# Performance work log

Hardware: AMD Instinct MI355X
Metric: run time of the kernel (lower is better)

## Reference

```python
import jax, jax.numpy as jnp
import numpy as np

B, C_LOCAL, C_GUIDE, C2, H, W = 16, 256, 256, 256, 64, 64
MID = C2 // 2          # mlp hidden channels
CQ = C_LOCAL // 4      # offset_gen hidden channels (also = groups)
EPS = 1e-5             # BatchNorm eps (inference mode)


def _conv(x, w, pad=0, groups=1, b=None):
    out = jax.lax.conv_general_dilated(
        x, w, window_strides=(1, 1), padding=((pad, pad), (pad, pad)),
        dimension_numbers=('NCHW', 'OIHW', 'NCHW'), feature_group_count=groups)
    if b is not None:
        out = out + b[None, :, None, None]
    return out


def _bn(x, g, b, m, v):
    scale = g / jnp.sqrt(v + EPS)
    return x * scale[None, :, None, None] + (b - m * scale)[None, :, None, None]


def _grid_sample(img, grid):
    # img: [C,H,W]; grid: [H,W,2] with (x,y) in [-1,1]; bilinear, zeros padding,
    # align_corners=False (pixel = ((g+1)*size - 1)/2)
    C, Hh, Ww = img.shape
    ix = (grid[..., 0] + 1.0) * (Ww * 0.5) - 0.5
    iy = (grid[..., 1] + 1.0) * (Hh * 0.5) - 0.5
    x0 = jnp.floor(ix); y0 = jnp.floor(iy)
    x1 = x0 + 1.0;      y1 = y0 + 1.0
    wx1 = ix - x0; wx0 = 1.0 - wx1
    wy1 = iy - y0; wy0 = 1.0 - wy1

    def gather(xi, yi):
        valid = (xi >= 0) & (xi < Ww) & (yi >= 0) & (yi < Hh)
        xc = jnp.clip(xi, 0, Ww - 1).astype(jnp.int32)
        yc = jnp.clip(yi, 0, Hh - 1).astype(jnp.int32)
        return img[:, yc, xc] * valid.astype(img.dtype)[None]  # [C,H,W]

    return (gather(x0, y0) * (wx0 * wy0)[None]
            + gather(x1, y0) * (wx1 * wy0)[None]
            + gather(x0, y1) * (wx0 * wy1)[None]
            + gather(x1, y1) * (wx1 * wy1)[None])


def setup_inputs() -> dict:
    key = jax.random.key(0)
    ks = jax.random.split(key, 20)
    w = lambda k, s: jax.random.normal(k, s, jnp.float32) * 0.05
    return {
        'x_local': jax.random.normal(ks[0], (B, C_LOCAL, H, W), jnp.float32),
        'x_guide': jax.random.normal(ks[1], (B, C_GUIDE, H, W), jnp.float32),
        'w_align': w(ks[2], (C2, C_GUIDE, 1, 1)),
        'bn1_g': 1.0 + 0.1 * jax.random.normal(ks[3], (C2,), jnp.float32),
        'bn1_b': 0.1 * jax.random.normal(ks[4], (C2,), jnp.float32),
        'bn1_m': 0.1 * jax.random.normal(ks[5], (C2,), jnp.float32),
        'bn1_v': 0.5 + jax.random.uniform(ks[6], (C2,), jnp.float32),
        'w_off1': w(ks[7], (CQ, 4, 3, 3)),   # grouped: in-ch per group = C_LOCAL/CQ = 4
        'w_off2': w(ks[8], (2, CQ, 1, 1)),
        'b_off2': 0.1 * jax.random.normal(ks[9], (2,), jnp.float32),
        'w_mlp1': w(ks[10], (MID, C_LOCAL, 1, 1)),
        'bn2_g': 1.0 + 0.1 * jax.random.normal(ks[11], (MID,), jnp.float32),
        'bn2_b': 0.1 * jax.random.normal(ks[12], (MID,), jnp.float32),
        'bn2_m': 0.1 * jax.random.normal(ks[13], (MID,), jnp.float32),
        'bn2_v': 0.5 + jax.random.uniform(ks[14], (MID,), jnp.float32),
        'w_mlp2': w(ks[15], (C2, MID, 1, 1)),
    }


def reference(x_local, x_guide, w_align, bn1_g, bn1_b, bn1_m, bn1_v,
              w_off1, w_off2, b_off2, w_mlp1, bn2_g, bn2_b, bn2_m, bn2_v,
              w_mlp2):
    # align(x_guide): 1x1 conv + BN
    g = _bn(_conv(x_guide, w_align), bn1_g, bn1_b, bn1_m, bn1_v)
    # offset_gen(x_local): grouped 3x3 conv -> SiLU -> 1x1 conv (bias) -> [B,2,H,W]
    off = _conv(x_local, w_off1, pad=1, groups=CQ)
    off = _conv(jax.nn.silu(off), w_off2, b=b_off2)
    # base grid in [-1,1], (x,y) last
    ys = jnp.linspace(-1.0, 1.0, H)
    xs = jnp.linspace(-1.0, 1.0, W)
    gy, gx = jnp.meshgrid(ys, xs, indexing='ij')
    base = jnp.stack((gx, gy), axis=-1)                      # [H,W,2]
    v_grid = base[None] + off.transpose(0, 2, 3, 1) * (2.0 / max(H, W))
    g_aligned = jax.vmap(_grid_sample)(g, v_grid)            # [B,C2,H,W]
    # mlp(x_local): 1x1 conv -> BN -> GELU(exact) -> 1x1 conv
    l = _conv(x_local, w_mlp1)
    l = jax.nn.gelu(_bn(l, bn2_g, bn2_b, bn2_m, bn2_v), approximate=False)
    l = _conv(l, w_mlp2)
    return jax.nn.silu(g_aligned + l)
```

## Files before the change

### kernel.cpp

```cpp
#include <hip/hip_runtime.h>

typedef unsigned short u16;
typedef __bf16 bf16x8 __attribute__((ext_vector_type(8)));
typedef float f32x4 __attribute__((ext_vector_type(4)));
typedef u16 u16x2 __attribute__((ext_vector_type(2)));
typedef u16 u16x4 __attribute__((ext_vector_type(4)));
typedef u16 u16x8 __attribute__((ext_vector_type(8)));

#define EPS 1e-5f

__device__ __forceinline__ u16 f2bf(float f) {
  unsigned u = __builtin_bit_cast(unsigned, f);
  u += 0x7FFFu + ((u >> 16) & 1u);
  return (u16)(u >> 16);
}
__device__ __forceinline__ float bf2f(u16 h) {
  unsigned u = ((unsigned)h) << 16;
  return __builtin_bit_cast(float, u);
}

__global__ void prep_weights(
    const float* __restrict__ wa, const float* __restrict__ g1, const float* __restrict__ b1,
    const float* __restrict__ m1, const float* __restrict__ v1,
    const float* __restrict__ w1, const float* __restrict__ g2, const float* __restrict__ b2,
    const float* __restrict__ m2, const float* __restrict__ v2,
    const float* __restrict__ w2,
    u16* __restrict__ Acat, u16* __restrict__ w1_o,
    float* __restrict__ bias1, float* __restrict__ bias2) {
  int c = blockIdx.x, k = threadIdx.x;
  float s1 = g1[c] / sqrtf(v1[c] + EPS);
  if (k < 256) Acat[c * 384 + k] = f2bf(wa[c * 256 + k] * s1);
  else         Acat[c * 384 + k] = f2bf(w2[c * 128 + (k - 256)]);
  if (c < 128) {
    float s2 = g2[c] / sqrtf(v2[c] + EPS);
    if (k < 256) w1_o[c * 256 + k] = f2bf(w1[c * 256 + k] * s2);
    if (k == 256) bias2[c] = b2[c] - m2[c] * s2;
  }
  if (k == 0) bias1[c] = b1[c] - m1[c] * s1;
}

__global__ __launch_bounds__(256) void gconv_kernel(
    const float* __restrict__ xl, const float* __restrict__ w1,
    u16* __restrict__ sbuf) {
  __shared__ float tile[4][18][66];
  const int tid = threadIdx.x;
  const int band = blockIdx.x;
  const int q = blockIdx.y;
  const int b = blockIdx.z;
  const float* xb = xl + ((size_t)b * 256 + 4 * q) * 4096;
  for (int i = tid; i < 4 * 18 * 66; i += 256) {
    int ci = i / (18 * 66);
    int rem = i - ci * (18 * 66);
    int r = rem / 66, c = rem - r * 66;
    int gy = band * 16 - 1 + r, gx = c - 1;
    float v = 0.f;
    if ((unsigned)gy < 64u && (unsigned)gx < 64u)
      v = xb[(size_t)ci * 4096 + gy * 64 + gx];
    tile[ci][r][c] = v;
  }
  float wq[36];
#pragma unroll
  for (int i = 0; i < 36; ++i) wq[i] = w1[q * 36 + i];
  __syncthreads();
  const int c = tid & 63, r0 = tid >> 6;
  u16* sp = sbuf + ((size_t)(b * 64 + q)) * 4096 + band * 1024;
#pragma unroll
  for (int k = 0; k < 4; ++k) {
    int r = r0 * 4 + k;
    float s = 0.f;
#pragma unroll
    for (int ci = 0; ci < 4; ++ci)
#pragma unroll
      for (int dy = 0; dy < 3; ++dy)
#pragma unroll
        for (int dx = 0; dx < 3; ++dx)
          s += wq[ci * 9 + dy * 3 + dx] * tile[ci][r + dy][c + dx];
    sp[r * 64 + c] = f2bf(s / (1.f + __expf(-s)));
  }
}

__global__ __launch_bounds__(256) void coords_kernel(
    const u16* __restrict__ sbuf, const float* __restrict__ w2,
    const float* __restrict__ b2, float* __restrict__ coords,
    float* __restrict__ wsum) {
  __shared__ float sw2[128];
  const int tid = threadIdx.x;
  if (tid < 128) sw2[tid] = w2[tid];
  __syncthreads();
  const int b = blockIdx.y;
  const int p = blockIdx.x * 256 + tid;
  const u16* sp = sbuf + (size_t)b * 64 * 4096 + p;
  float ax = 0.f, ay = 0.f;
#pragma unroll 8
  for (int q = 0; q < 64; ++q) {
    float v = bf2f(sp[(size_t)q * 4096]);
    ax += sw2[q] * v;
    ay += sw2[64 + q] * v;
  }
  int y = p >> 6, x = p & 63;
  float ix = (64.f / 63.f) * (float)x + ax + b2[0] - 0.5f;
  float iy = (64.f / 63.f) * (float)y + ay + b2[1] - 0.5f;
  ((float2*)coords)[(size_t)b * 4096 + p] = make_float2(ix, iy);
  float x0f = floorf(ix), y0f = floorf(iy);
  int x0 = (int)x0f, y0 = (int)y0f;
  float wx1 = ix - x0f, wx0 = 1.f - wx1;
  float wy1 = iy - y0f, wy0 = 1.f - wy1;
  bool vx0 = (unsigned)x0 < 64u, vx1 = (unsigned)(x0 + 1) < 64u;
  bool vy0 = (unsigned)y0 < 64u, vy1 = (unsigned)(y0 + 1) < 64u;
  float s = (vx0 && vy0 ? wx0 * wy0 : 0.f) + (vx1 && vy0 ? wx1 * wy0 : 0.f) +
            (vx0 && vy1 ? wx0 * wy1 : 0.f) + (vx1 && vy1 ? wx1 * wy1 : 0.f);
  wsum[(size_t)b * 4096 + p] = s;
}

__global__ __launch_bounds__(256) void sampler_kernel(
    const float* __restrict__ xg, const float* __restrict__ coords,
    u16* __restrict__ xgs) {
  const int wg = blockIdx.x;
  const int id = (wg & 7) * 512 + (wg >> 3);
  const int kq = id >> 10;
  const int b = (id >> 6) & 15, row = id & 63;
  const int px = threadIdx.x & 63, ko = threadIdx.x >> 6;
  const int p = row * 64 + px;
  float2 cd = ((const float2*)coords)[(size_t)b * 4096 + p];
  float ix = cd.x, iy = cd.y;
  float x0f = floorf(ix), y0f = floorf(iy);
  int x0 = (int)x0f, y0 = (int)y0f;
  float wx1 = ix - x0f, wx0 = 1.f - wx1;
  float wy1 = iy - y0f, wy0 = 1.f - wy1;
  bool vx0 = (unsigned)x0 < 64u, vx1 = (unsigned)(x0 + 1) < 64u;
  bool vy0 = (unsigned)y0 < 64u, vy1 = (unsigned)(y0 + 1) < 64u;
  int x0c = min(max(x0, 0), 63), x1c = min(max(x0 + 1, 0), 63);
  int y0c = min(max(y0, 0), 63), y1c = min(max(y0 + 1, 0), 63);
  float w00 = (vx0 && vy0) ? wx0 * wy0 : 0.f;
  float w10 = (vx1 && vy0) ? wx1 * wy0 : 0.f;
  float w01 = (vx0 && vy1) ? wx0 * wy1 : 0.f;
  float w11 = (vx1 && vy1) ? wx1 * wy1 : 0.f;
  const int i00 = y0c * 64 + x0c, i10 = y0c * 64 + x1c;
  const int i01 = y1c * 64 + x0c, i11 = y1c * 64 + x1c;
  const int k0 = kq * 64 + ko * 16;
  const float* bb = xg + ((size_t)b * 256 + k0) * 4096;
  u16* xo = xgs + ((size_t)b * 256 + k0) * 4096 + p;
#pragma unroll
  for (int kk = 0; kk < 16; ++kk) {
    const float* bp = bb + (size_t)kk * 4096;
    float v = w00 * bp[i00] + w10 * bp[i10] + w01 * bp[i01] + w11 * bp[i11];
    xo[(size_t)kk * 4096] = f2bf(v);
  }
}

__global__ __launch_bounds__(256, 2) void gemm_h(
    const u16* __restrict__ A, const float* __restrict__ Bsrc,
    u16* __restrict__ Out, const float* __restrict__ bias) {
  __shared__ u16 Al[128][40];
  __shared__ u16 Bl[128][40];
  const int tid = threadIdx.x;
  const int b = blockIdx.y;
  const int n0 = blockIdx.x * 128;
  const int wave = tid >> 6, lane = tid & 63;
  const int wr = wave >> 1, wc = wave & 1;
  const int lr = lane & 15, kg = lane >> 4;
  f32x4 acc[4][4] = {};
  const float* Bf = Bsrc + (size_t)b * 256 * 4096;

  for (int kt = 0; kt < 8; ++kt) {
    {
      int m = tid >> 1, pos = (tid & 1) * 16;
      u16x8 v0 = *(const u16x8*)(A + (size_t)m * 256 + kt * 32 + pos);
      u16x8 v1 = *(const u16x8*)(A + (size_t)m * 256 + kt * 32 + pos + 8);
      *(u16x8*)&Al[m][pos] = v0;
      *(u16x8*)&Al[m][pos + 8] = v1;
    }
    {
      int nq = tid & 31, kq = tid >> 5;
      int kb = kt * 32 + kq * 4;
      int nb = n0 + nq * 4;
      f32x4 r[4];
#pragma unroll
      for (int i = 0; i < 4; ++i)
        r[i] = *(const f32x4*)(Bf + (size_t)(kb + i) * 4096 + nb);
#pragma unroll
      for (int j = 0; j < 4; ++j) {
        u16x4 w = {f2bf(r[0][j]), f2bf(r[1][j]), f2bf(r[2][j]), f2bf(r[3][j])};
        *(u16x4*)&Bl[nq * 4 + j][kq * 4] = w;
      }
    }
    __syncthreads();
    bf16x8 af[4], bfr[4];
#pragma unroll
    for (int i = 0; i < 4; ++i) {
      af[i] = *(const bf16x8*)&Al[wr * 64 + i * 16 + lr][kg * 8];
      bfr[i] = *(const bf16x8*)&Bl[wc * 64 + i * 16 + lr][kg * 8];
    }
#pragma unroll
    for (int i = 0; i < 4; ++i)
#pragma unroll
      for (int j = 0; j < 4; ++j)
        acc[i][j] = __builtin_amdgcn_mfma_f32_16x16x32_bf16(af[i], bfr[j], acc[i][j], 0, 0, 0);
    __syncthreads();
  }
  u16* O = Out + (size_t)b * 4096 * 128;
#pragma unroll
  for (int i = 0; i < 4; ++i) {
    int rb = wr * 64 + i * 16 + kg * 4;
    f32x4 b4 = *(const f32x4*)(bias + rb);
#pragma unroll
    for (int j = 0; j < 4; ++j) {
      int col = n0 + wc * 64 + j * 16 + lr;
      u16x4 w;
#pragma unroll
      for (int e = 0; e < 4; ++e) {
        float v = acc[i][j][e] + b4[e];
        v = 0.5f * v * (1.f + erff(v * 0.70710678118f));
        w[e] = f2bf(v);
      }
      *(u16x4*)(O + (size_t)col * 128 + rb) = w;
    }
  }
}

__global__ __launch_bounds__(512, 2) void gemm_final(
    const u16* __restrict__ A,
    const u16* __restrict__ xgs,
    const u16* __restrict__ hb,
    const float* __restrict__ bias1, const float* __restrict__ wsum,
    float* __restrict__ out) {
  __shared__ u16 Al[256][40];
  __shared__ u16 Bl[128][40];
  const int tid = threadIdx.x;
  const int b = blockIdx.y;
  const int n0 = blockIdx.x * 128;
  const int wave = tid >> 6, lane = tid & 63;
  const int wr = wave >> 1, wc = wave & 1;
  const int lr = lane & 15, kg = lane >> 4;
  f32x4 acc[4][4] = {};
  const u16* xb = xgs + (size_t)b * 256 * 4096;
  const u16* hp = hb + (size_t)b * 4096 * 128;

  for (int kt = 0; kt < 12; ++kt) {
#pragma unroll
    for (int c = 0; c < 2; ++c) {
      int ch = tid + c * 512;
      int m = ch >> 2, pos = (ch & 3) * 8;
      *(u16x8*)&Al[m][pos] = *(const u16x8*)(A + (size_t)m * 384 + kt * 32 + pos);
    }
    if (kt < 8) {
      int kq2 = tid >> 5;
      int nq = tid & 31;
      int k0 = kt * 32 + kq2 * 2;
      u16x4 r0 = *(const u16x4*)(xb + (size_t)k0 * 4096 + n0 + nq * 4);
      u16x4 r1 = *(const u16x4*)(xb + (size_t)(k0 + 1) * 4096 + n0 + nq * 4);
#pragma unroll
      for (int j = 0; j < 4; ++j) {
        u16x2 w = {r0[j], r1[j]};
        *(u16x2*)&Bl[nq * 4 + j][kq2 * 2] = w;
      }
    } else {
      int pl = tid >> 2, kq = tid & 3;
      *(u16x8*)&Bl[pl][kq * 8] =
          *(const u16x8*)(hp + (size_t)(n0 + pl) * 128 + (kt - 8) * 32 + kq * 8);
    }
    __syncthreads();
    bf16x8 af[4], bfr[4];
#pragma unroll
    for (int i = 0; i < 4; ++i) {
      af[i] = *(const bf16x8*)&Al[wr * 64 + i * 16 + lr][kg * 8];
      bfr[i] = *(const bf16x8*)&Bl[wc * 64 + i * 16 + lr][kg * 8];
    }
#pragma unroll
    for (int i = 0; i < 4; ++i)
#pragma unroll
      for (int j = 0; j < 4; ++j)
        acc[i][j] = __builtin_amdgcn_mfma_f32_16x16x32_bf16(af[i], bfr[j], acc[i][j], 0, 0, 0);
    __syncthreads();
  }

  float* Ob = out + (size_t)b * 256 * 4096;
#pragma unroll
  for (int j = 0; j < 4; ++j) {
    int col = n0 + wc * 64 + j * 16 + lr;
    float ws = wsum[(size_t)b * 4096 + col];
#pragma unroll
    for (int i = 0; i < 4; ++i) {
      int rb = wr * 64 + i * 16 + kg * 4;
      f32x4 b4 = *(const f32x4*)(bias1 + rb);
#pragma unroll
      for (int e = 0; e < 4; ++e) {
        float v = acc[i][j][e] + b4[e] * ws;
        Ob[(size_t)(rb + e) * 4096 + col] = v / (1.f + __expf(-v));
      }
    }
  }
}

extern "C" void kernel_launch(void* const* d_in, const int* in_sizes, int n_in,
                              void* d_out, int out_size, void* d_ws, size_t ws_size,
                              hipStream_t stream) {
  const float* x_local = (const float*)d_in[0];
  const float* x_guide = (const float*)d_in[1];
  const float* w_align = (const float*)d_in[2];
  const float* bn1_g = (const float*)d_in[3];
  const float* bn1_b = (const float*)d_in[4];
  const float* bn1_m = (const float*)d_in[5];
  const float* bn1_v = (const float*)d_in[6];
  const float* w_off1 = (const float*)d_in[7];
  const float* w_off2 = (const float*)d_in[8];
  const float* b_off2 = (const float*)d_in[9];
  const float* w_mlp1 = (const float*)d_in[10];
  const float* bn2_g = (const float*)d_in[11];
  const float* bn2_b = (const float*)d_in[12];
  const float* bn2_m = (const float*)d_in[13];
  const float* bn2_v = (const float*)d_in[14];
  const float* w_mlp2 = (const float*)d_in[15];

  char* ws = (char*)d_ws;
  u16* Acat = (u16*)(ws + 0);
  u16* w1_bf = (u16*)(ws + 196608);
  float* bias1 = (float*)(ws + 262144);
  float* bias2 = (float*)(ws + 263168);
  float* wsum = (float*)(ws + 263680);
  float* coords = (float*)(ws + 525824);
  u16* xgs = (u16*)(ws + 1050112);
  u16* hbuf = (u16*)(ws + 34604544);
  u16* sbuf = hbuf;

  prep_weights<<<256, 384, 0, stream>>>(
      w_align, bn1_g, bn1_b, bn1_m, bn1_v,
      w_mlp1, bn2_g, bn2_b, bn2_m, bn2_v, w_mlp2,
      Acat, w1_bf, bias1, bias2);

  gconv_kernel<<<dim3(4, 64, 16), 256, 0, stream>>>(x_local, w_off1, sbuf);

  coords_kernel<<<dim3(16, 16), 256, 0, stream>>>(sbuf, w_off2, b_off2, coords, wsum);

  sampler_kernel<<<4096, 256, 0, stream>>>(x_guide, coords, xgs);

  gemm_h<<<dim3(32, 16), 256, 0, stream>>>(w1_bf, x_local, hbuf, bias2);

  gemm_final<<<dim3(32, 16), 512, 0, stream>>>(Acat, xgs, hbuf, bias1, wsum, (float*)d_out);
}
```

Baseline: 130.3 us.

## Store sampled guide and MLP hidden in a shared pixel-major K-concatenated buffer

New measurement: 133.9 us. 2.7% more time.

```diff
diff --git a/kernel.cpp b/kernel.cpp
--- a/kernel.cpp
+++ b/kernel.cpp
@@ -3,7 +3,6 @@
 typedef unsigned short u16;
 typedef __bf16 bf16x8 __attribute__((ext_vector_type(8)));
 typedef float f32x4 __attribute__((ext_vector_type(4)));
-typedef u16 u16x2 __attribute__((ext_vector_type(2)));
 typedef u16 u16x4 __attribute__((ext_vector_type(4)));
 typedef u16 u16x8 __attribute__((ext_vector_type(8)));
 
@@ -114,12 +113,12 @@
 
 __global__ __launch_bounds__(256) void sampler_kernel(
     const float* __restrict__ xg, const float* __restrict__ coords,
-    u16* __restrict__ xgs) {
+    u16* __restrict__ xh) {
   const int wg = blockIdx.x;
   const int id = (wg & 7) * 512 + (wg >> 3);
   const int kq = id >> 10;
   const int b = (id >> 6) & 15, row = id & 63;
-  const int px = threadIdx.x & 63, ko = threadIdx.x >> 6;
+  const int px = threadIdx.x >> 2, ko = threadIdx.x & 3;
   const int p = row * 64 + px;
   float2 cd = ((const float2*)coords)[(size_t)b * 4096 + p];
   float ix = cd.x, iy = cd.y;
@@ -139,18 +138,21 @@
   const int i01 = y1c * 64 + x0c, i11 = y1c * 64 + x1c;
   const int k0 = kq * 64 + ko * 16;
   const float* bb = xg + ((size_t)b * 256 + k0) * 4096;
-  u16* xo = xgs + ((size_t)b * 256 + k0) * 4096 + p;
+  u16 o[16];
 #pragma unroll
   for (int kk = 0; kk < 16; ++kk) {
     const float* bp = bb + (size_t)kk * 4096;
     float v = w00 * bp[i00] + w10 * bp[i10] + w01 * bp[i01] + w11 * bp[i11];
-    xo[(size_t)kk * 4096] = f2bf(v);
-  }
+    o[kk] = f2bf(v);
+  }
+  u16* xo = xh + ((size_t)b * 4096 + p) * 384 + k0;
+  *(u16x8*)(xo) = *(u16x8*)&o[0];
+  *(u16x8*)(xo + 8) = *(u16x8*)&o[8];
 }
 
 __global__ __launch_bounds__(256, 2) void gemm_h(
     const u16* __restrict__ A, const float* __restrict__ Bsrc,
-    u16* __restrict__ Out, const float* __restrict__ bias) {
+    u16* __restrict__ xh, const float* __restrict__ bias) {
   __shared__ u16 Al[128][40];
   __shared__ u16 Bl[128][40];
   const int tid = threadIdx.x;
@@ -198,7 +200,7 @@
         acc[i][j] = __builtin_amdgcn_mfma_f32_16x16x32_bf16(af[i], bfr[j], acc[i][j], 0, 0, 0);
     __syncthreads();
   }
-  u16* O = Out + (size_t)b * 4096 * 128;
+  u16* O = xh + (size_t)b * 4096 * 384 + 256;
 #pragma unroll
   for (int i = 0; i < 4; ++i) {
     int rb = wr * 64 + i * 16 + kg * 4;
@@ -213,51 +215,38 @@
         v = 0.5f * v * (1.f + erff(v * 0.70710678118f));
         w[e] = f2bf(v);
       }
-      *(u16x4*)(O + (size_t)col * 128 + rb) = w;
-    }
-  }
-}
-
-__global__ __launch_bounds__(512, 2) void gemm_final(
+      *(u16x4*)(O + (size_t)col * 384 + rb) = w;
+    }
+  }
+}
+
+__global__ __launch_bounds__(256) void gemm_final(
     const u16* __restrict__ A,
-    const u16* __restrict__ xgs,
-    const u16* __restrict__ hb,
+    const u16* __restrict__ xh,
     const float* __restrict__ bias1, const float* __restrict__ wsum,
     float* __restrict__ out) {
-  __shared__ u16 Al[256][40];
+  __shared__ u16 Al[128][40];
   __shared__ u16 Bl[128][40];
   const int tid = threadIdx.x;
-  const int b = blockIdx.y;
-  const int n0 = blockIdx.x * 128;
+  const int wg = blockIdx.y * 64 + blockIdx.x;
+  const int nmb = (wg & 7) * 128 + (wg >> 3);
+  const int m = nmb & 1;
+  const int n0 = ((nmb >> 1) & 31) * 128;
+  const int b = nmb >> 6;
   const int wave = tid >> 6, lane = tid & 63;
   const int wr = wave >> 1, wc = wave & 1;
   const int lr = lane & 15, kg = lane >> 4;
   f32x4 acc[4][4] = {};
-  const u16* xb = xgs + (size_t)b * 256 * 4096;
-  const u16* hp = hb + (size_t)b * 4096 * 128;
+  const u16* Ab = A + (size_t)m * 128 * 384;
+  const u16* Bb = xh + ((size_t)b * 4096 + n0) * 384;
 
   for (int kt = 0; kt < 12; ++kt) {
 #pragma unroll
     for (int c = 0; c < 2; ++c) {
-      int ch = tid + c * 512;
-      int m = ch >> 2, pos = (ch & 3) * 8;
-      *(u16x8*)&Al[m][pos] = *(const u16x8*)(A + (size_t)m * 384 + kt * 32 + pos);
-    }
-    if (kt < 8) {
-      int kq2 = tid >> 5;
-      int nq = tid & 31;
-      int k0 = kt * 32 + kq2 * 2;
-      u16x4 r0 = *(const u16x4*)(xb + (size_t)k0 * 4096 + n0 + nq * 4);
-      u16x4 r1 = *(const u16x4*)(xb + (size_t)(k0 + 1) * 4096 + n0 + nq * 4);
-#pragma unroll
-      for (int j = 0; j < 4; ++j) {
-        u16x2 w = {r0[j], r1[j]};
-        *(u16x2*)&Bl[nq * 4 + j][kq2 * 2] = w;
-      }
-    } else {
-      int pl = tid >> 2, kq = tid & 3;
-      *(u16x8*)&Bl[pl][kq * 8] =
-          *(const u16x8*)(hp + (size_t)(n0 + pl) * 128 + (kt - 8) * 32 + kq * 8);
+      int ch = tid + c * 256;
+      int r = ch >> 2, pos = (ch & 3) * 8;
+      *(u16x8*)&Al[r][pos] = *(const u16x8*)(Ab + (size_t)r * 384 + kt * 32 + pos);
+      *(u16x8*)&Bl[r][pos] = *(const u16x8*)(Bb + (size_t)r * 384 + kt * 32 + pos);
     }
     __syncthreads();
     bf16x8 af[4], bfr[4];
@@ -281,7 +270,7 @@
     float ws = wsum[(size_t)b * 4096 + col];
 #pragma unroll
     for (int i = 0; i < 4; ++i) {
-      int rb = wr * 64 + i * 16 + kg * 4;
+      int rb = m * 128 + wr * 64 + i * 16 + kg * 4;
       f32x4 b4 = *(const f32x4*)(bias1 + rb);
 #pragma unroll
       for (int e = 0; e < 4; ++e) {
@@ -319,9 +308,8 @@
   float* bias2 = (float*)(ws + 263168);
   float* wsum = (float*)(ws + 263680);
   float* coords = (float*)(ws + 525824);
-  u16* xgs = (u16*)(ws + 1050112);
-  u16* hbuf = (u16*)(ws + 34604544);
-  u16* sbuf = hbuf;
+  u16* xh = (u16*)(ws + 1050112);
+  u16* sbuf = xh;
 
   prep_weights<<<256, 384, 0, stream>>>(
       w_align, bn1_g, bn1_b, bn1_m, bn1_v,
@@ -332,9 +320,9 @@
 
   coords_kernel<<<dim3(16, 16), 256, 0, stream>>>(sbuf, w_off2, b_off2, coords, wsum);
 
-  sampler_kernel<<<4096, 256, 0, stream>>>(x_guide, coords, xgs);
-
-  gemm_h<<<dim3(32, 16), 256, 0, stream>>>(w1_bf, x_local, hbuf, bias2);
-
-  gemm_final<<<dim3(32, 16), 512, 0, stream>>>(Acat, xgs, hbuf, bias1, wsum, (float*)d_out);
-}
+  sampler_kernel<<<4096, 256, 0, stream>>>(x_guide, coords, xh);
+
+  gemm_h<<<dim3(32, 16), 256, 0, stream>>>(w1_bf, x_local, xh, bias2);
+
+  gemm_final<<<dim3(64, 16), 256, 0, stream>>>(Acat, xh, bias1, wsum, (float*)d_out);
+}
```
